# Performance work log

Hardware: AMD Instinct MI355X
Metric: run time of the kernel (lower is better)

## Reference

```python
import jax, jax.numpy as jnp
import numpy as np

TEMPERATURE = 0.07
NUM_NEGATIVES = 128
B, C, H, W = 4, 256, 32, 32
N_TOTAL = B * H * W  # 4096


def setup_inputs() -> dict:
    key = jax.random.key(0)
    k1, k2, k3 = jax.random.split(key, 3)
    feat_q = jax.random.normal(k1, (B, C, H, W), dtype=jnp.float32)
    feat_k = jax.random.normal(k2, (B, C, H, W), dtype=jnp.float32)
    # uniform draws in [0, N_TOTAL-1): same distribution as indexing into the
    # length-(N-1) 'choices' array in the original per-i loop
    neg_indices = jax.random.randint(k3, (N_TOTAL, NUM_NEGATIVES), 0, N_TOTAL - 1, dtype=jnp.int64 if jax.config.jax_enable_x64 else jnp.int32)
    return {"feat_q": feat_q, "feat_k": feat_k, "neg_indices": neg_indices}


def reference(feat_q, feat_k, neg_indices):
    b, c, h, w = feat_q.shape
    n = b * h * w
    q = feat_q.reshape(b, c, -1)
    k = feat_k.reshape(b, c, -1)
    # F.normalize(dim=1), eps=1e-12
    q = q / jnp.maximum(jnp.linalg.norm(q, axis=1, keepdims=True), 1e-12)
    k = k / jnp.maximum(jnp.linalg.norm(k, axis=1, keepdims=True), 1e-12)
    q = q.transpose(0, 2, 1).reshape(-1, c)  # [N, C]
    k = k.transpose(0, 2, 1).reshape(-1, c)  # [N, C]
    l_pos = jnp.sum(q * k, axis=1, keepdims=True)  # [N, 1]
    # self-exclusion: choices = all_idx without i -> shift sampled idx >= i up by 1
    row = jnp.arange(n, dtype=neg_indices.dtype)[:, None]
    idx = neg_indices + (neg_indices >= row).astype(neg_indices.dtype)  # [N, K]
    k_neg = k[idx]  # [N, K, C] gather
    l_neg = jnp.einsum('nc,nkc->nk', q, k_neg)  # [N, K]
    logits = jnp.concatenate([l_pos, l_neg], axis=1) / TEMPERATURE  # [N, 1+K]
    # cross-entropy with label 0 for every row
    loss = jnp.mean(jax.nn.logsumexp(logits, axis=1) - logits[:, 0])
    return loss
```

## Files before the change

### kernel.cpp

```cpp
#include <hip/hip_runtime.h>
#include <hip/hip_bf16.h>

#define N_TOTAL 4096
#define C_DIM 256
#define K_NEG 128
#define HW 1024
#define TEMP_INV (1.0f / 0.07f)

typedef _Float16 h8 __attribute__((ext_vector_type(8)));
typedef float fv2 __attribute__((ext_vector_type(2)));

__global__ __launch_bounds__(256) void norm_tr_kernel(
    const float* __restrict__ fq, const float* __restrict__ fk,
    _Float16* __restrict__ qh, unsigned char* __restrict__ kh8) {
  const int bid = blockIdx.x;
  const int tensor = bid >> 8;
  const int chunk = bid & 255;
  const int n0 = chunk * 16;
  const int b = n0 / HW, s0 = n0 % HW;
  const float* base = (tensor ? fk : fq) + (size_t)b * C_DIM * HW + s0;

  const int t = threadIdx.x;
  __shared__ float tile[16][C_DIM + 1];
  __shared__ float red[16][17];
  __shared__ float sinv[16];

  {
    const float* src = base + (size_t)t * HW;
#pragma unroll
    for (int p = 0; p < 4; ++p) {
      const float4 v = *(const float4*)(src + p * 4);
      tile[p * 4 + 0][t] = v.x;
      tile[p * 4 + 1][t] = v.y;
      tile[p * 4 + 2][t] = v.z;
      tile[p * 4 + 3][t] = v.w;
    }
  }
  __syncthreads();

  {
    const int s = t & 15, cg = t >> 4;
    float acc = 0.f;
#pragma unroll
    for (int i = 0; i < 16; ++i) {
      float v = tile[s][cg * 16 + i];
      acc = fmaf(v, v, acc);
    }
    red[s][cg] = acc;
  }
  __syncthreads();
  if (t < 16) {
    float tot = 0.f;
#pragma unroll
    for (int g = 0; g < 16; ++g) tot += red[t][g];
    const float scale_extra = tensor ? 1.0f : TEMP_INV;
    sinv[t] = scale_extra / fmaxf(sqrtf(tot), 1e-12f);
  }
  __syncthreads();

  if (tensor == 0) {
    const int s = t & 15, c16 = t >> 4;
    const float inv = sinv[s];
    h8 o0, o1;
#pragma unroll
    for (int j = 0; j < 8; ++j) o0[j] = (_Float16)(tile[s][c16 * 16 + j] * inv);
#pragma unroll
    for (int j = 0; j < 8; ++j)
      o1[j] = (_Float16)(tile[s][c16 * 16 + 8 + j] * inv);
    h8* dst = (h8*)(qh + (size_t)(n0 + s) * C_DIM + c16 * 16);
    dst[0] = o0;
    dst[1] = o1;
  } else {
    const int s = t >> 4, c16 = t & 15;
    const float inv = sinv[s];
    uint4 W;
#pragma unroll
    for (int p = 0; p < 4; ++p) {
      const int e = c16 * 16 + p * 4;
      unsigned u = 0;
      u = __builtin_amdgcn_cvt_pk_fp8_f32(tile[s][e + 0] * inv,
                                          tile[s][e + 1] * inv, u, false);
      u = __builtin_amdgcn_cvt_pk_fp8_f32(tile[s][e + 2] * inv,
                                          tile[s][e + 3] * inv, u, true);
      ((unsigned*)&W)[p] = u;
    }
    ((uint4*)(kh8 + (size_t)(n0 + s) * C_DIM))[c16] = W;
  }
}

__global__ __launch_bounds__(256) void nce_kernel(
    const _Float16* __restrict__ qh, const unsigned char* __restrict__ kh8,
    const int* __restrict__ neg, float* __restrict__ loss_buf) {
  const int n = blockIdx.x;
  const int t = threadIdx.x;
  const int lane = t & 63;
  const int w = t >> 6;
  const int sub = lane & 7;
  const int unit = w * 8 + (lane >> 3);

  __shared__ float sneg[K_NEG];
  __shared__ float s_lpos;

  int r[4];
#pragma unroll
  for (int j = 0; j < 4; ++j) {
    int x = neg[(size_t)n * K_NEG + j * 32 + unit];
    r[j] = x + (x >= n ? 1 : 0);
  }
  const h8* qrow = (const h8*)(qh + (size_t)n * C_DIM);
  h8 qv[4];
  qv[0] = qrow[2 * sub];
  qv[1] = qrow[2 * sub + 1];
  qv[2] = qrow[16 + 2 * sub];
  qv[3] = qrow[16 + 2 * sub + 1];
  float qf[32];
#pragma unroll
  for (int i = 0; i < 4; ++i)
#pragma unroll
    for (int e = 0; e < 8; ++e) qf[i * 8 + e] = (float)qv[i][e];

  uint4 kp[2];
  if (unit == 0) {
    const uint4* kr = (const uint4*)(kh8 + (size_t)n * C_DIM);
    kp[0] = kr[sub];
    kp[1] = kr[8 + sub];
  }
  uint4 kd[4][2];
#pragma unroll
  for (int j = 0; j < 4; ++j) {
    const uint4* kr = (const uint4*)(kh8 + (size_t)r[j] * C_DIM);
    kd[j][0] = kr[sub];
    kd[j][1] = kr[8 + sub];
  }

  auto dot16 = [&](const uint4& U, int base, float& acc) {
#pragma unroll
    for (int p = 0; p < 4; ++p) {
      const unsigned u = ((const unsigned*)&U)[p];
      fv2 ab = __builtin_amdgcn_cvt_pk_f32_fp8(u, false);
      fv2 cd = __builtin_amdgcn_cvt_pk_f32_fp8(u, true);
      acc = fmaf(ab.x, qf[base + p * 4 + 0], acc);
      acc = fmaf(ab.y, qf[base + p * 4 + 1], acc);
      acc = fmaf(cd.x, qf[base + p * 4 + 2], acc);
      acc = fmaf(cd.y, qf[base + p * 4 + 3], acc);
    }
  };

#pragma unroll
  for (int j = 0; j < 4; ++j) {
    float acc = 0.f;
    dot16(kd[j][0], 0, acc);
    dot16(kd[j][1], 16, acc);
    acc += __shfl_xor(acc, 1);
    acc += __shfl_xor(acc, 2);
    acc += __shfl_xor(acc, 4);
    if (sub == 0) sneg[j * 32 + unit] = acc;
  }
  if (unit == 0) {
    float acc = 0.f;
    dot16(kp[0], 0, acc);
    dot16(kp[1], 16, acc);
    acc += __shfl_xor(acc, 1);
    acc += __shfl_xor(acc, 2);
    acc += __shfl_xor(acc, 4);
    if (sub == 0) s_lpos = acc;
  }
  __syncthreads();

  if (w == 0) {
    float lp = s_lpos;
    float x1 = sneg[lane];
    float x2 = sneg[lane + 64];
    float m = fmaxf(fmaxf(x1, x2), lp);
#pragma unroll
    for (int off = 32; off; off >>= 1) m = fmaxf(m, __shfl_xor(m, off));
    float s = __expf(x1 - m) + __expf(x2 - m);
#pragma unroll
    for (int off = 32; off; off >>= 1) s += __shfl_xor(s, off);
    if (lane == 0) loss_buf[n] = m + __logf(s) - lp;
  }
}

__global__ __launch_bounds__(1024) void reduce_kernel(
    const float* __restrict__ loss_buf, float* __restrict__ out) {
  const int t = threadIdx.x;
  const float4 v = ((const float4*)loss_buf)[t];
  float s = (v.x + v.y) + (v.z + v.w);
#pragma unroll
  for (int off = 32; off; off >>= 1) s += __shfl_xor(s, off);
  __shared__ float red[16];
  if ((t & 63) == 0) red[t >> 6] = s;
  __syncthreads();
  if (t < 16) {
    float x = red[t];
#pragma unroll
    for (int off = 8; off; off >>= 1) x += __shfl_xor(x, off);
    if (t == 0) out[0] = x * (1.0f / N_TOTAL);
  }
}

extern "C" void kernel_launch(void* const* d_in, const int* in_sizes, int n_in,
                              void* d_out, int out_size, void* d_ws,
                              size_t ws_size, hipStream_t stream) {
  const float* fq = (const float*)d_in[0];
  const float* fk = (const float*)d_in[1];
  const int* neg = (const int*)d_in[2];
  float* out = (float*)d_out;

  _Float16* qh = (_Float16*)d_ws;
  unsigned char* kh8 = (unsigned char*)(qh + (size_t)N_TOTAL * C_DIM);
  float* loss_buf = (float*)(kh8 + (size_t)N_TOTAL * C_DIM);

  hipLaunchKernelGGL(norm_tr_kernel, dim3(512), dim3(256), 0, stream,
                     fq, fk, qh, kh8);
  hipLaunchKernelGGL(nce_kernel, dim3(N_TOTAL), dim3(256), 0, stream,
                     qh, kh8, neg, loss_buf);
  hipLaunchKernelGGL(reduce_kernel, dim3(1), dim3(1024), 0, stream,
                     loss_buf, out);
}
```

Baseline: 79.57 us.

## Map one wavefront per row with online softmax and fuse final reduction via atomics

Restructures the NCE kernel so each wavefront handles a whole row: eight 8-lane units each loop over 16 negatives and keep a running max and sum, merged across lanes by shuffles. This removes the shared-memory staging and the block-wide sync per row. The separate reduce kernel is dropped; each block does an atomicAdd into the output, which norm_tr_kernel zeroes first, saving one launch. In exchange there is less memory-level parallelism per row, since gathers are now issued in a loop instead of all up front, and the summation order becomes nondeterministic.

```diff
diff --git a/kernel.cpp b/kernel.cpp
--- a/kernel.cpp
+++ b/kernel.cpp
@@ -12,7 +12,10 @@
 
 __global__ __launch_bounds__(256) void norm_tr_kernel(
     const float* __restrict__ fq, const float* __restrict__ fk,
-    _Float16* __restrict__ qh, unsigned char* __restrict__ kh8) {
+    _Float16* __restrict__ qh, unsigned char* __restrict__ kh8,
+    float* __restrict__ out) {
+  if (blockIdx.x == 0 && threadIdx.x == 0) out[0] = 0.f;
+
   const int bid = blockIdx.x;
   const int tensor = bid >> 8;
   const int chunk = bid & 255;
@@ -88,25 +91,17 @@
   }
 }
 
-__global__ __launch_bounds__(256) void nce_kernel(
+__global__ __launch_bounds__(1024) void nce_kernel(
     const _Float16* __restrict__ qh, const unsigned char* __restrict__ kh8,
-    const int* __restrict__ neg, float* __restrict__ loss_buf) {
-  const int n = blockIdx.x;
+    const int* __restrict__ neg, float* __restrict__ out) {
   const int t = threadIdx.x;
-  const int lane = t & 63;
-  const int w = t >> 6;
+  const int w = t >> 6, lane = t & 63;
   const int sub = lane & 7;
-  const int unit = w * 8 + (lane >> 3);
-
-  __shared__ float sneg[K_NEG];
-  __shared__ float s_lpos;
-
-  int r[4];
-#pragma unroll
-  for (int j = 0; j < 4; ++j) {
-    int x = neg[(size_t)n * K_NEG + j * 32 + unit];
-    r[j] = x + (x >= n ? 1 : 0);
-  }
+  const int unit = lane >> 3;
+  const int n = blockIdx.x * 16 + w;
+
+  __shared__ float wloss[16];
+
   const h8* qrow = (const h8*)(qh + (size_t)n * C_DIM);
   h8 qv[4];
   qv[0] = qrow[2 * sub];
@@ -119,19 +114,8 @@
 #pragma unroll
     for (int e = 0; e < 8; ++e) qf[i * 8 + e] = (float)qv[i][e];
 
-  uint4 kp[2];
-  if (unit == 0) {
-    const uint4* kr = (const uint4*)(kh8 + (size_t)n * C_DIM);
-    kp[0] = kr[sub];
-    kp[1] = kr[8 + sub];
-  }
-  uint4 kd[4][2];
-#pragma unroll
-  for (int j = 0; j < 4; ++j) {
-    const uint4* kr = (const uint4*)(kh8 + (size_t)r[j] * C_DIM);
-    kd[j][0] = kr[sub];
-    kd[j][1] = kr[8 + sub];
-  }
+  const uint4* kpr = (const uint4*)(kh8 + (size_t)n * C_DIM);
+  uint4 kp0 = kpr[sub], kp1 = kpr[8 + sub];
 
   auto dot16 = [&](const uint4& U, int base, float& acc) {
 #pragma unroll
@@ -146,56 +130,55 @@
     }
   };
 
-#pragma unroll
-  for (int j = 0; j < 4; ++j) {
+  const int* nrow = neg + (size_t)n * K_NEG + unit * 16;
+
+  float m = -1e30f, s = 0.f;
+#pragma unroll 2
+  for (int j = 0; j < 16; ++j) {
+    const int x = nrow[j];
+    const int r = x + (x >= n ? 1 : 0);
+    const uint4* kr = (const uint4*)(kh8 + (size_t)r * C_DIM);
+    const uint4 k0 = kr[sub], k1 = kr[8 + sub];
     float acc = 0.f;
-    dot16(kd[j][0], 0, acc);
-    dot16(kd[j][1], 16, acc);
+    dot16(k0, 0, acc);
+    dot16(k1, 16, acc);
     acc += __shfl_xor(acc, 1);
     acc += __shfl_xor(acc, 2);
     acc += __shfl_xor(acc, 4);
-    if (sub == 0) sneg[j * 32 + unit] = acc;
-  }
-  if (unit == 0) {
+    const float mn = fmaxf(m, acc);
+    s = s * __expf(m - mn) + __expf(acc - mn);
+    m = mn;
+  }
+
+  float lp;
+  {
     float acc = 0.f;
-    dot16(kp[0], 0, acc);
-    dot16(kp[1], 16, acc);
+    dot16(kp0, 0, acc);
+    dot16(kp1, 16, acc);
     acc += __shfl_xor(acc, 1);
     acc += __shfl_xor(acc, 2);
     acc += __shfl_xor(acc, 4);
-    if (sub == 0) s_lpos = acc;
-  }
-  __syncthreads();
-
-  if (w == 0) {
-    float lp = s_lpos;
-    float x1 = sneg[lane];
-    float x2 = sneg[lane + 64];
-    float m = fmaxf(fmaxf(x1, x2), lp);
-#pragma unroll
-    for (int off = 32; off; off >>= 1) m = fmaxf(m, __shfl_xor(m, off));
-    float s = __expf(x1 - m) + __expf(x2 - m);
-#pragma unroll
-    for (int off = 32; off; off >>= 1) s += __shfl_xor(s, off);
-    if (lane == 0) loss_buf[n] = m + __logf(s) - lp;
-  }
-}
-
-__global__ __launch_bounds__(1024) void reduce_kernel(
-    const float* __restrict__ loss_buf, float* __restrict__ out) {
-  const int t = threadIdx.x;
-  const float4 v = ((const float4*)loss_buf)[t];
-  float s = (v.x + v.y) + (v.z + v.w);
-#pragma unroll
-  for (int off = 32; off; off >>= 1) s += __shfl_xor(s, off);
-  __shared__ float red[16];
-  if ((t & 63) == 0) red[t >> 6] = s;
-  __syncthreads();
+    lp = acc;
+  }
+
+#pragma unroll
+  for (int off = 8; off <= 32; off <<= 1) {
+    const float mo = __shfl_xor(m, off);
+    const float so = __shfl_xor(s, off);
+    const float mn = fmaxf(m, mo);
+    s = s * __expf(m - mn) + so * __expf(mo - mn);
+    m = mn;
+  }
+  const float M = fmaxf(m, lp);
+  const float stot = s * __expf(m - M) + __expf(lp - M);
+  if (lane == 0) wloss[w] = M + __logf(stot) - lp;
+  __syncthreads();
+
   if (t < 16) {
-    float x = red[t];
-#pragma unroll
-    for (int off = 8; off; off >>= 1) x += __shfl_xor(x, off);
-    if (t == 0) out[0] = x * (1.0f / N_TOTAL);
+    float v = wloss[t];
+#pragma unroll
+    for (int off = 8; off; off >>= 1) v += __shfl_xor(v, off);
+    if (t == 0) atomicAdd(out, v * (1.0f / N_TOTAL));
   }
 }
 
@@ -209,12 +192,9 @@
 
   _Float16* qh = (_Float16*)d_ws;
   unsigned char* kh8 = (unsigned char*)(qh + (size_t)N_TOTAL * C_DIM);
-  float* loss_buf = (float*)(kh8 + (size_t)N_TOTAL * C_DIM);
 
   hipLaunchKernelGGL(norm_tr_kernel, dim3(512), dim3(256), 0, stream,
-                     fq, fk, qh, kh8);
-  hipLaunchKernelGGL(nce_kernel, dim3(N_TOTAL), dim3(256), 0, stream,
-                     qh, kh8, neg, loss_buf);
-  hipLaunchKernelGGL(reduce_kernel, dim3(1), dim3(1024), 0, stream,
-                     loss_buf, out);
+                     fq, fk, qh, kh8, out);
+  hipLaunchKernelGGL(nce_kernel, dim3(N_TOTAL / 16), dim3(1024), 0, stream,
+                     qh, kh8, neg, out);
 }
```

Measured after the change: 80.19 us. About the same (+0.8%).
